# Kernel tuning notes

Measured on AMD Instinct MI355X. Metric: run time of the kernel, lower is better.

## Reference

```python
import jax, jax.numpy as jnp
import numpy as np

EPS = 1e-6      # fast_transformers LinearAttention eps
LN_EPS = 1e-5   # torch LayerNorm default
L_LAYERS = 4
N_HEADS = 16
D_MODEL = 1024
D_FF = 4096


def _layernorm(x, g, b):
    mu = jnp.mean(x, axis=-1, keepdims=True)
    var = jnp.mean(jnp.square(x - mu), axis=-1, keepdims=True)
    return (x - mu) * jax.lax.rsqrt(var + LN_EPS) * g + b


def _layer(x, fmask, Wq, bq, Wk, bk, Wv, bv, Wo, bo, W1, b1, W2, b2, g1, be1, g2, be2):
    N, S, D = x.shape
    H = N_HEADS
    d = D // H
    q = (x @ Wq.T + bq).reshape(N, S, H, d)
    k = (x @ Wk.T + bk).reshape(N, S, H, d)
    v = (x @ Wv.T + bv).reshape(N, S, H, d)
    # feature map: elu(x) + 1
    Q = jax.nn.elu(q) + 1.0
    K = (jax.nn.elu(k) + 1.0) * fmask[:, :, None, None]
    # non-causal linear attention
    KV = jnp.einsum('nshd,nshm->nhmd', K, v)                       # [N,H,d,d]
    Z = 1.0 / (jnp.einsum('nlhd,nhd->nlh', Q, K.sum(axis=1)) + EPS)
    attn = jnp.einsum('nlhd,nhmd,nlh->nlhm', Q, KV, Z).reshape(N, S, D)
    x = x + (attn @ Wo.T + bo)
    y = x = _layernorm(x, g1, be1)
    y = jax.nn.gelu(y @ W1.T + b1, approximate=False) @ W2.T + b2
    return _layernorm(x + y, g2, be2)


def setup_inputs() -> dict:
    key = jax.random.key(0)
    ks = jax.random.split(key, 12)
    N, S, D, F = 4, 4096, D_MODEL, D_FF
    L = L_LAYERS
    s = 0.02
    inp = {
        'src': jax.random.normal(ks[0], (N, S, D), dtype=jnp.float32),
        'src_key_padding_mask': jnp.zeros((N, S), dtype=bool),
        'Wq': jax.random.normal(ks[1], (L, D, D), dtype=jnp.float32) * s,
        'bq': jnp.zeros((L, D), dtype=jnp.float32),
        'Wk': jax.random.normal(ks[2], (L, D, D), dtype=jnp.float32) * s,
        'bk': jnp.zeros((L, D), dtype=jnp.float32),
        'Wv': jax.random.normal(ks[3], (L, D, D), dtype=jnp.float32) * s,
        'bv': jnp.zeros((L, D), dtype=jnp.float32),
        'Wo': jax.random.normal(ks[4], (L, D, D), dtype=jnp.float32) * s,
        'bo': jnp.zeros((L, D), dtype=jnp.float32),
        'W1': jax.random.normal(ks[5], (L, F, D), dtype=jnp.float32) * s,
        'b1': jnp.zeros((L, F), dtype=jnp.float32),
        'W2': jax.random.normal(ks[6], (L, D, F), dtype=jnp.float32) * s,
        'b2': jnp.zeros((L, D), dtype=jnp.float32),
        'g1': jnp.ones((L, D), dtype=jnp.float32),
        'be1': jnp.zeros((L, D), dtype=jnp.float32),
        'g2': jnp.ones((L, D), dtype=jnp.float32),
        'be2': jnp.zeros((L, D), dtype=jnp.float32),
    }
    return inp


def reference(src, src_key_padding_mask, Wq, bq, Wk, bk, Wv, bv, Wo, bo,
              W1, b1, W2, b2, g1, be1, g2, be2):
    N, S, D = src.shape
    # LengthMask: valid positions are the first (S - num_paddings) tokens
    actual_len = S - src_key_padding_mask.sum(axis=1)              # [N]
    fmask = (jnp.arange(S)[None, :] < actual_len[:, None]).astype(src.dtype)
    x = src
    for i in range(L_LAYERS):
        x = _layer(x, fmask, Wq[i], bq[i], Wk[i], bk[i], Wv[i], bv[i],
                   Wo[i], bo[i], W1[i], b1[i], W2[i], b2[i],
                   g1[i], be1[i], g2[i], be2[i])
    return x
```

## Files before the change

kernel.cpp:

```cpp
#include <hip/hip_runtime.h>
#include <cstdint>

typedef unsigned short ushort_t;
typedef short v8s __attribute__((ext_vector_type(8)));
typedef float v4f __attribute__((ext_vector_type(4)));
typedef unsigned short v4u __attribute__((ext_vector_type(4)));

#define DMODEL 1024
#define DFF 4096
#define SEQ 4096
#define NBATCH 4
#define NHEAD 16
#define HDIM 64
#define NLAYER 4
#define MTOK (NBATCH*SEQ)

#define EPI_QKV 0
#define EPI_RES 3
#define EPI_GELU 4

__device__ __forceinline__ float bf2f(ushort_t u) {
    unsigned v = ((unsigned)u) << 16; float f; __builtin_memcpy(&f, &v, 4); return f;
}
__device__ __forceinline__ ushort_t f2bf(float f) {
    unsigned u; __builtin_memcpy(&u, &f, 4);
    u = (u + 0x7fffu + ((u >> 16) & 1u)) >> 16;
    return (ushort_t)u;
}

__device__ __forceinline__ float gelu_f(float x) {
    const float y = x * 0.70710678118f;
    const float ay = fabsf(y);
    const float t = __builtin_amdgcn_rcpf(1.f + 0.3275911f * ay);
    const float p = t * (0.254829592f + t * (-0.284496736f + t * (1.421413741f +
                    t * (-1.453152027f + t * 1.061405429f))));
    const float e = __expf(-y * y);
    float er = 1.f - p * e;
    er = (y < 0.f) ? -er : er;
    return 0.5f * x * (1.f + er);
}

__global__ __launch_bounds__(256) void cvt_bf16(const float* __restrict__ in,
                                                ushort_t* __restrict__ out, int n) {
    int i = (blockIdx.x * 256 + threadIdx.x) * 4;
    if (i >= n) return;
    float4 v = *(const float4*)(in + i);
    v4u o;
    o[0] = f2bf(v.x); o[1] = f2bf(v.y); o[2] = f2bf(v.z); o[3] = f2bf(v.w);
    *(v4u*)(out + i) = o;
}

__global__ __launch_bounds__(256) void cvt_qkv(const float* __restrict__ Wq,
                                               const float* __restrict__ Wk,
                                               const float* __restrict__ Wv,
                                               ushort_t* __restrict__ out) {
    const size_t DD = (size_t)DMODEL * DMODEL;
    size_t i = ((size_t)blockIdx.x * 256 + threadIdx.x) * 4;
    int l = (int)(i / DD);
    size_t r = i % DD;
    const float* srcs[3] = { Wq + l * DD + r, Wk + l * DD + r, Wv + l * DD + r };
    #pragma unroll
    for (int s = 0; s < 3; s++) {
        float4 v = *(const float4*)srcs[s];
        v4u o;
        o[0] = f2bf(v.x); o[1] = f2bf(v.y); o[2] = f2bf(v.z); o[3] = f2bf(v.w);
        *(v4u*)(out + ((size_t)l * 3 + s) * DD + r) = o;
    }
}

__global__ __launch_bounds__(256) void lens_kernel(const unsigned char* __restrict__ mask,
                                                   int* __restrict__ lens) {
    int lane = threadIdx.x & 63, w = threadIdx.x >> 6;
    int cnt = 0;
    for (int i = lane; i < SEQ; i += 64) cnt += (mask[w * SEQ + i] != 0) ? 1 : 0;
    #pragma unroll
    for (int off = 32; off; off >>= 1) cnt += __shfl_down(cnt, off);
    if (lane == 0) lens[w] = SEQ - cnt;
}

template <int EPI>
__global__ __launch_bounds__(256) void gemm_bt(
    const ushort_t* __restrict__ A, const ushort_t* __restrict__ B,
    const float* __restrict__ bias, const float* __restrict__ bias2,
    const float* __restrict__ bias3, const float* res,
    const int* __restrict__ lens,
    ushort_t* __restrict__ outB, ushort_t* __restrict__ outB2,
    ushort_t* __restrict__ outB3, float* outF,
    int M, int N, int K)
{
    __shared__ __align__(16) ushort_t As[128 * 64];
    __shared__ __align__(16) ushort_t Bs[128 * 64];

    const int tid = threadIdx.x;
    const int lane = tid & 63;
    const int wave = tid >> 6;
    const int nb = N >> 7;
    const int xcd = blockIdx.x & 7;
    const int q = blockIdx.x >> 3;
    const int bm = (q / nb) * 8 + xcd;
    const int bn = q % nb;
    const int wm = (wave >> 1) * 64;
    const int wn = (wave & 1) * 64;
    const int lr = lane & 15;
    const int lq = lane >> 4;

    v4f acc[4][4];
    #pragma unroll
    for (int i = 0; i < 4; i++)
        #pragma unroll
        for (int j = 0; j < 4; j++) acc[i][j] = (v4f)0.f;

    const int srow = tid >> 3;
    const int schunk = (tid & 7) ^ (srow & 7);
    const ushort_t* Ag = A + (size_t)(bm * 128 + srow) * K + schunk * 8;
    const ushort_t* Bg = B + (size_t)(bn * 128 + srow) * K + schunk * 8;
    ushort_t* Asp = As + tid * 8;
    ushort_t* Bsp = Bs + tid * 8;
    const size_t rstep = (size_t)32 * K;

    int a_off[2][4], b_off[2][4];
    #pragma unroll
    for (int h = 0; h < 2; h++)
        #pragma unroll
        for (int i = 0; i < 4; i++) {
            const int ra = wm + i * 16 + lr;
            a_off[h][i] = ra * 64 + (((h * 4 + lq) ^ (ra & 7)) * 8);
            const int rb = wn + i * 16 + lr;
            b_off[h][i] = rb * 64 + (((h * 4 + lq) ^ (rb & 7)) * 8);
        }

    for (int k0 = 0; k0 < K; k0 += 64) {
        #pragma unroll
        for (int i = 0; i < 4; i++)
            __builtin_amdgcn_global_load_lds((const void*)(Ag + i * rstep + k0),
                                             (void*)(Asp + i * 2048), 16, 0, 0);
        #pragma unroll
        for (int i = 0; i < 4; i++)
            __builtin_amdgcn_global_load_lds((const void*)(Bg + i * rstep + k0),
                                             (void*)(Bsp + i * 2048), 16, 0, 0);
        __syncthreads();

        #pragma unroll
        for (int h = 0; h < 2; h++) {
            v8s af[4], bfr[4];
            #pragma unroll
            for (int i = 0; i < 4; i++) af[i] = *(const v8s*)&As[a_off[h][i]];
            #pragma unroll
            for (int j = 0; j < 4; j++) bfr[j] = *(const v8s*)&Bs[b_off[h][j]];
            #pragma unroll
            for (int i = 0; i < 4; i++)
                #pragma unroll
                for (int j = 0; j < 4; j++)
                    acc[i][j] = __builtin_amdgcn_mfma_f32_16x16x32_bf16(af[i], bfr[j], acc[i][j], 0, 0, 0);
        }
        __syncthreads();
    }

    const int row0 = bm * 128 + wm + lq * 4;
    const int col0 = bn * 128 + wn + lr;

    const int seg = bn >> 3;
    ushort_t* qkv_out = (EPI == EPI_QKV)
        ? (seg == 0 ? outB : (seg == 1 ? outB2 : outB3)) : outB;
    const float* qkv_bias = (EPI == EPI_QKV)
        ? (seg == 0 ? bias : (seg == 1 ? bias2 : bias3)) : bias;
    const int blen = (EPI == EPI_QKV) ? lens[bm >> 5] : 0;

    #pragma unroll
    for (int i = 0; i < 4; i++) {
        #pragma unroll
        for (int j = 0; j < 4; j++) {
            const int gn = col0 + j * 16;
            const float bsv = (EPI == EPI_QKV) ? qkv_bias[gn & 1023] : bias[gn];
            #pragma unroll
            for (int r = 0; r < 4; r++) {
                const int gm = row0 + i * 16 + r;
                float v = acc[i][j][r] + bsv;
                if (EPI == EPI_QKV) {
                    const size_t oi = (size_t)gm * DMODEL + (gn & 1023);
                    if (seg == 2) {
                        qkv_out[oi] = f2bf(v);
                    } else {
                        float e = v > 0.f ? v + 1.f : __expf(v);
                        if (seg == 1 && (gm & 4095) >= blen) e = 0.f;
                        qkv_out[oi] = f2bf(e);
                    }
                } else if (EPI == EPI_RES) {
                    const size_t oi = (size_t)gm * N + gn;
                    outF[oi] = v + res[oi];
                } else {
                    const size_t oi = (size_t)gm * N + gn;
                    __builtin_nontemporal_store(f2bf(gelu_f(v)), &outB[oi]);
                }
            }
        }
    }
}

__global__ __launch_bounds__(256) void ksum_kernel(const ushort_t* __restrict__ K,
                                                   float* __restrict__ out) {
    const int blk = blockIdx.x;
    const int n = blk >> 4, cg = blk & 15;
    const int tx = threadIdx.x & 63, ty = threadIdx.x >> 6;
    const int col = cg * 64 + tx;
    const ushort_t* p = K + ((size_t)n * SEQ + ty * 1024) * DMODEL + col;
    float a = 0.f;
    for (int s = 0; s < 1024; s++) a += bf2f(p[(size_t)s * DMODEL]);
    __shared__ float red[4][64];
    red[ty][tx] = a;
    __syncthreads();
    if (ty == 0) out[n * DMODEL + col] = red[0][tx] + red[1][tx] + red[2][tx] + red[3][tx];
}

__global__ __launch_bounds__(256) void kv_part(const ushort_t* __restrict__ K,
                                               const ushort_t* __restrict__ V,
                                               float* __restrict__ part) {
    const int chunk = blockIdx.x, nh = blockIdx.y;
    const int n = nh >> 4, h = nh & 15;
    const int tid = threadIdx.x;
    const int tm = tid >> 4, td = tid & 15;
    __shared__ float Ks[16][68];
    __shared__ float Vs[16][68];
    float acc[4][4] = {};
    const int s0 = chunk * 512;
    for (int sb = 0; sb < 512; sb += 16) {
        __syncthreads();
        for (int idx = tid; idx < 1024; idx += 256) {
            const int r = idx >> 6, c = idx & 63;
            const size_t gpos = ((size_t)(n * SEQ + s0 + sb + r)) * DMODEL + h * HDIM + c;
            Ks[r][c] = bf2f(K[gpos]);
            Vs[r][c] = bf2f(V[gpos]);
        }
        __syncthreads();
        #pragma unroll
        for (int s = 0; s < 16; s++) {
            float kv[4], vv[4];
            #pragma unroll
            for (int j = 0; j < 4; j++) kv[j] = Ks[s][td * 4 + j];
            #pragma unroll
            for (int i = 0; i < 4; i++) vv[i] = Vs[s][tm * 4 + i];
            #pragma unroll
            for (int i = 0; i < 4; i++)
                #pragma unroll
                for (int j = 0; j < 4; j++)
                    acc[i][j] += vv[i] * kv[j];
        }
    }
    float* o = part + ((size_t)chunk * 64 + nh) * 4096;
    #pragma unroll
    for (int i = 0; i < 4; i++)
        #pragma unroll
        for (int j = 0; j < 4; j++)
            o[(tm * 4 + i) * 64 + td * 4 + j] = acc[i][j];
}

__global__ __launch_bounds__(256) void kv_reduce(const float* __restrict__ part,
                                                 float* __restrict__ KV) {
    const int gid = blockIdx.x * 256 + threadIdx.x;
    float a = 0.f;
    #pragma unroll
    for (int c = 0; c < 8; c++) a += part[(size_t)c * (64 * 4096) + gid];
    KV[gid] = a;
}

__global__ __launch_bounds__(256) void attn_kernel(const ushort_t* __restrict__ Q,
                                                   const float* __restrict__ KV,
                                                   const float* __restrict__ Ksum,
                                                   ushort_t* __restrict__ out) {
    const int bx = blockIdx.x, nh = blockIdx.y;
    const int n = nh >> 4, h = nh & 15;
    const int tid = threadIdx.x;
    const int ty = tid >> 4, tx = tid & 15;
    __shared__ float KVs[64][65];
    __shared__ float Qs[64][65];
    __shared__ float Zs[64];
    const int t0 = n * SEQ + bx * 64;
    for (int idx = tid; idx < 4096; idx += 256) {
        const int r = idx >> 6, c = idx & 63;
        KVs[r][c] = KV[(size_t)nh * 4096 + idx];
        Qs[r][c] = bf2f(Q[((size_t)(t0 + r)) * DMODEL + h * HDIM + c]);
    }
    __syncthreads();
    if (tid < 64) {
        const float* ks = Ksum + n * DMODEL + h * HDIM;
        float a = 0.f;
        #pragma unroll
        for (int d = 0; d < 64; d++) a += Qs[tid][d] * ks[d];
        Zs[tid] = 1.f / (a + 1e-6f);
    }
    __syncthreads();
    float acc[4][4] = {};
    for (int d = 0; d < 64; d++) {
        float qv[4], kv[4];
        #pragma unroll
        for (int i = 0; i < 4; i++) qv[i] = Qs[ty * 4 + i][d];
        #pragma unroll
        for (int j = 0; j < 4; j++) kv[j] = KVs[tx * 4 + j][d];
        #pragma unroll
        for (int i = 0; i < 4; i++)
            #pragma unroll
            for (int j = 0; j < 4; j++)
                acc[i][j] += qv[i] * kv[j];
    }
    #pragma unroll
    for (int i = 0; i < 4; i++) {
        const int r = ty * 4 + i;
        const float z = Zs[r];
        v4u o;
        #pragma unroll
        for (int j = 0; j < 4; j++) o[j] = f2bf(acc[i][j] * z);
        *(v4u*)&out[((size_t)(t0 + r)) * DMODEL + h * HDIM + tx * 4] = o;
    }
}

__global__ __launch_bounds__(256) void ln_kernel(const float* in, float* outF,
                                                 ushort_t* outB,
                                                 const float* __restrict__ g,
                                                 const float* __restrict__ b) {
    const int row = blockIdx.x;
    const int tid = threadIdx.x;
    const float4 v = ((const float4*)(in + (size_t)row * DMODEL))[tid];
    float s = v.x + v.y + v.z + v.w;
    float ss = v.x * v.x + v.y * v.y + v.z * v.z + v.w * v.w;
    #pragma unroll
    for (int off = 32; off; off >>= 1) {
        s += __shfl_down(s, off);
        ss += __shfl_down(ss, off);
    }
    __shared__ float red[8];
    const int lane = tid & 63, w = tid >> 6;
    if (lane == 0) { red[w * 2] = s; red[w * 2 + 1] = ss; }
    __syncthreads();
    s = red[0] + red[2] + red[4] + red[6];
    ss = red[1] + red[3] + red[5] + red[7];
    const float mu = s * (1.f / DMODEL);
    const float var = ss * (1.f / DMODEL) - mu * mu;
    const float rs = rsqrtf(var + 1e-5f);
    const float4 gg = ((const float4*)g)[tid];
    const float4 bb = ((const float4*)b)[tid];
    float4 o;
    o.x = (v.x - mu) * rs * gg.x + bb.x;
    o.y = (v.y - mu) * rs * gg.y + bb.y;
    o.z = (v.z - mu) * rs * gg.z + bb.z;
    o.w = (v.w - mu) * rs * gg.w + bb.w;
    ((float4*)(outF + (size_t)row * DMODEL))[tid] = o;
    if (outB) {
        v4u ob;
        ob[0] = f2bf(o.x); ob[1] = f2bf(o.y); ob[2] = f2bf(o.z); ob[3] = f2bf(o.w);
        *(v4u*)(outB + (size_t)row * DMODEL + tid * 4) = ob;
    }
}

extern "C" void kernel_launch(void* const* d_in, const int* in_sizes, int n_in,
                              void* d_out, int out_size, void* d_ws, size_t ws_size,
                              hipStream_t stream) {
    const float* src = (const float*)d_in[0];
    const unsigned char* mask = (const unsigned char*)d_in[1];
    const float* Wq = (const float*)d_in[2];
    const float* bq = (const float*)d_in[3];
    const float* Wk = (const float*)d_in[4];
    const float* bk = (const float*)d_in[5];
    const float* Wv = (const float*)d_in[6];
    const float* bv = (const float*)d_in[7];
    const float* Wo = (const float*)d_in[8];
    const float* bo = (const float*)d_in[9];
    const float* W1 = (const float*)d_in[10];
    const float* b1 = (const float*)d_in[11];
    const float* W2 = (const float*)d_in[12];
    const float* b2 = (const float*)d_in[13];
    const float* g1 = (const float*)d_in[14];
    const float* be1 = (const float*)d_in[15];
    const float* g2 = (const float*)d_in[16];
    const float* be2 = (const float*)d_in[17];

    float* xout = (float*)d_out;

    char* ws = (char*)d_ws;
    size_t off = 0;
    auto alloc = [&](size_t bytes) -> void* {
        void* p = (void*)(ws + off);
        off += (bytes + 255) & ~(size_t)255;
        return p;
    };
    const size_t DD = (size_t)DMODEL * DMODEL;
    const size_t FD = (size_t)DFF * DMODEL;
    const size_t MD = (size_t)MTOK * DMODEL;

    ushort_t* wqkv_bf = (ushort_t*)alloc(NLAYER * 3 * DD * 2);
    ushort_t* wo_bf = (ushort_t*)alloc(NLAYER * DD * 2);
    ushort_t* w1r = (ushort_t*)alloc(FD * 2);
    ushort_t* w2r = (ushort_t*)alloc(FD * 2);
    ushort_t* xbf = (ushort_t*)alloc(MD * 2);
    ushort_t* Qb = (ushort_t*)alloc(MD * 2);
    ushort_t* Kb = (ushort_t*)alloc(MD * 2);
    ushort_t* Vb = (ushort_t*)alloc(MD * 2);
    (void)alloc(MD * 2);
    ushort_t* hb = Qb;
    float* Ksum = (float*)alloc((size_t)NBATCH * DMODEL * 4);
    float* KVp = (float*)alloc((size_t)8 * 64 * 4096 * 4);
    float* KVb = (float*)alloc((size_t)64 * 4096 * 4);
    int* lens = (int*)alloc(256);
    if (off > ws_size) return;

    cvt_qkv<<<dim3((unsigned)((NLAYER * DD) / 1024)), dim3(256), 0, stream>>>(Wq, Wk, Wv, wqkv_bf);
    cvt_bf16<<<dim3((unsigned)((NLAYER * DD) / 1024)), dim3(256), 0, stream>>>(Wo, wo_bf, (int)(NLAYER * DD));
    lens_kernel<<<dim3(1), dim3(256), 0, stream>>>(mask, lens);
    cvt_bf16<<<dim3((unsigned)(MD / 1024)), dim3(256), 0, stream>>>(src, xbf, (int)MD);

    const dim3 blk(256);
    const dim3 gQKV((MTOK / 128) * (3 * DMODEL / 128));
    const dim3 gD((MTOK / 128) * (DMODEL / 128));
    const dim3 gF((MTOK / 128) * (DFF / 128));

    for (int l = 0; l < NLAYER; l++) {
        const ushort_t* wqkvl = wqkv_bf + (size_t)l * 3 * DD;
        const ushort_t* wol = wo_bf + l * DD;
        const float* bql = bq + l * DMODEL;
        const float* bkl = bk + l * DMODEL;
        const float* bvl = bv + l * DMODEL;
        const float* bol = bo + l * DMODEL;
        const float* b1l = b1 + l * DFF;
        const float* b2l = b2 + l * DMODEL;
        const float* g1l = g1 + l * DMODEL;
        const float* be1l = be1 + l * DMODEL;
        const float* g2l = g2 + l * DMODEL;
        const float* be2l = be2 + l * DMODEL;
        const float* resx = (l == 0) ? src : xout;

        gemm_bt<EPI_QKV><<<gQKV, blk, 0, stream>>>(xbf, wqkvl, bql, bkl, bvl,
            nullptr, lens, Qb, Kb, Vb, nullptr, MTOK, 3 * DMODEL, DMODEL);

        ksum_kernel<<<dim3(64), blk, 0, stream>>>(Kb, Ksum);
        kv_part<<<dim3(8, 64), blk, 0, stream>>>(Kb, Vb, KVp);
        kv_reduce<<<dim3(64 * 4096 / 256), blk, 0, stream>>>(KVp, KVb);
        attn_kernel<<<dim3(64, 64), blk, 0, stream>>>(Qb, KVb, Ksum, Kb);

        gemm_bt<EPI_RES><<<gD, blk, 0, stream>>>(Kb, wol, bol, nullptr, nullptr,
            resx, lens, nullptr, nullptr, nullptr, xout, MTOK, DMODEL, DMODEL);
        ln_kernel<<<dim3(MTOK), blk, 0, stream>>>(xout, xout, xbf, g1l, be1l);

        cvt_bf16<<<dim3((unsigned)(FD / 1024)), blk, 0, stream>>>(W1 + l * FD, w1r, (int)FD);
        gemm_bt<EPI_GELU><<<gF, blk, 0, stream>>>(xbf, w1r, b1l, nullptr, nullptr,
            nullptr, lens, hb, nullptr, nullptr, nullptr, MTOK, DFF, DMODEL);
        cvt_bf16<<<dim3((unsigned)(FD / 1024)), blk, 0, stream>>>(W2 + l * FD, w2r, (int)FD);
        gemm_bt<EPI_RES><<<gD, blk, 0, stream>>>(hb, w2r, b2l, nullptr, nullptr,
            xout, lens, nullptr, nullptr, nullptr, xout, MTOK, DMODEL, DFF);
        ln_kernel<<<dim3(MTOK), blk, 0, stream>>>(xout, xout, (l == NLAYER - 1) ? nullptr : xbf, g2l, be2l);
    }
}
```

Before: 3.662 ms.

## Double-buffer GEMM shared tiles with register prefetch of next K slice

Replaces the direct global-to-LDS loads with register-staged loads into a two-slot LDS ring. The next K tile is fetched into registers while the current one is consumed, and one of the two barriers per iteration is removed. Launch bounds now request two blocks per CU, and the GELU epilogue switches from nontemporal to normal stores. This aims to overlap global memory latency with MFMA work, at the cost of more registers and double the LDS (64KB per block) and the loss of the async LDS-load path.

```diff
diff --git a/kernel.cpp b/kernel.cpp
--- a/kernel.cpp
+++ b/kernel.cpp
@@ -79,7 +79,7 @@
 }
 
 template <int EPI>
-__global__ __launch_bounds__(256) void gemm_bt(
+__global__ __launch_bounds__(256, 2) void gemm_bt(
     const ushort_t* __restrict__ A, const ushort_t* __restrict__ B,
     const float* __restrict__ bias, const float* __restrict__ bias2,
     const float* __restrict__ bias3, const float* res,
@@ -88,8 +88,8 @@
     ushort_t* __restrict__ outB3, float* outF,
     int M, int N, int K)
 {
-    __shared__ __align__(16) ushort_t As[128 * 64];
-    __shared__ __align__(16) ushort_t Bs[128 * 64];
+    __shared__ __align__(16) ushort_t As[2][128 * 64];
+    __shared__ __align__(16) ushort_t Bs[2][128 * 64];
 
     const int tid = threadIdx.x;
     const int lane = tid & 63;
@@ -114,9 +114,8 @@
     const int schunk = (tid & 7) ^ (srow & 7);
     const ushort_t* Ag = A + (size_t)(bm * 128 + srow) * K + schunk * 8;
     const ushort_t* Bg = B + (size_t)(bn * 128 + srow) * K + schunk * 8;
-    ushort_t* Asp = As + tid * 8;
-    ushort_t* Bsp = Bs + tid * 8;
     const size_t rstep = (size_t)32 * K;
+    const int sdst = tid * 8;
 
     int a_off[2][4], b_off[2][4];
     #pragma unroll
@@ -129,31 +128,41 @@
             b_off[h][i] = rb * 64 + (((h * 4 + lq) ^ (rb & 7)) * 8);
         }
 
-    for (int k0 = 0; k0 < K; k0 += 64) {
-        #pragma unroll
-        for (int i = 0; i < 4; i++)
-            __builtin_amdgcn_global_load_lds((const void*)(Ag + i * rstep + k0),
-                                             (void*)(Asp + i * 2048), 16, 0, 0);
-        #pragma unroll
-        for (int i = 0; i < 4; i++)
-            __builtin_amdgcn_global_load_lds((const void*)(Bg + i * rstep + k0),
-                                             (void*)(Bsp + i * 2048), 16, 0, 0);
+    v8s ra[4], rb[4];
+    #pragma unroll
+    for (int i = 0; i < 4; i++) ra[i] = *(const v8s*)(Ag + i * rstep);
+    #pragma unroll
+    for (int i = 0; i < 4; i++) rb[i] = *(const v8s*)(Bg + i * rstep);
+
+    const int iters = K >> 6;
+    int p = 0;
+    for (int t = 0; t < iters; ++t) {
+        #pragma unroll
+        for (int i = 0; i < 4; i++) *(v8s*)&As[p][sdst + i * 2048] = ra[i];
+        #pragma unroll
+        for (int i = 0; i < 4; i++) *(v8s*)&Bs[p][sdst + i * 2048] = rb[i];
+        if (t + 1 < iters) {
+            const int k0 = (t + 1) << 6;
+            #pragma unroll
+            for (int i = 0; i < 4; i++) ra[i] = *(const v8s*)(Ag + i * rstep + k0);
+            #pragma unroll
+            for (int i = 0; i < 4; i++) rb[i] = *(const v8s*)(Bg + i * rstep + k0);
+        }
         __syncthreads();
-
         #pragma unroll
         for (int h = 0; h < 2; h++) {
             v8s af[4], bfr[4];
             #pragma unroll
-            for (int i = 0; i < 4; i++) af[i] = *(const v8s*)&As[a_off[h][i]];
-            #pragma unroll
-            for (int j = 0; j < 4; j++) bfr[j] = *(const v8s*)&Bs[b_off[h][j]];
+            for (int i = 0; i < 4; i++) af[i] = *(const v8s*)&As[p][a_off[h][i]];
+            #pragma unroll
+            for (int j = 0; j < 4; j++) bfr[j] = *(const v8s*)&Bs[p][b_off[h][j]];
             #pragma unroll
             for (int i = 0; i < 4; i++)
                 #pragma unroll
                 for (int j = 0; j < 4; j++)
                     acc[i][j] = __builtin_amdgcn_mfma_f32_16x16x32_bf16(af[i], bfr[j], acc[i][j], 0, 0, 0);
         }
-        __syncthreads();
+        p ^= 1;
     }
 
     const int row0 = bm * 128 + wm + lq * 4;
@@ -190,7 +199,7 @@
                     outF[oi] = v + res[oi];
                 } else {
                     const size_t oi = (size_t)gm * N + gn;
-                    __builtin_nontemporal_store(f2bf(gelu_f(v)), &outB[oi]);
+                    outB[oi] = f2bf(gelu_f(v));
                 }
             }
         }
```

New measurement: 3.359 ms. 1.09x faster.
